# Performance work log

Hardware: AMD Instinct MI355X
Metric: run time of the kernel (lower is better)

Reference implementation:

```python
import jax, jax.numpy as jnp
import numpy as np

B, S, D, E, K = 4, 4096, 2048, 64, 2


def setup_inputs() -> dict:
    key = jax.random.key(0)
    k1, k2, k3 = jax.random.split(key, 3)
    x = jax.random.normal(k1, (B, S, D), dtype=jnp.float32)
    W = jax.random.normal(k2, (D, E), dtype=jnp.float32) / np.sqrt(D)
    b = jnp.zeros((E,), dtype=jnp.float32)
    noise = jax.random.normal(k3, (B, S, E), dtype=jnp.float32)
    return {"x": x, "W": W, "b": b, "noise": noise}


def reference(x, W, b, noise):
    # logits = Linear(x); noisy gating adds N(0,1)/10 noise
    logits = jnp.einsum('bsd,de->bse', x, W) + b  # [B,S,E]
    logits = logits + noise * 0.1
    scores = jax.nn.softmax(logits, axis=-1)      # [B,S,E]
    topk_scores, topk_indices = jax.lax.top_k(scores, K)  # [B,S,K]
    return topk_scores, topk_indices, scores
```

## Files before the change

### kernel.cpp

```cpp
#include <hip/hip_runtime.h>
#include <math.h>

#define BS_TOT 16384
#define DDIM   2048
#define NEXP   64
#define TOPK   2

#define NW   16
#define RPB  64
#define DS   (DDIM / NW)

__global__ __launch_bounds__(1024, 2)
void router_kernel(const float* __restrict__ x, const float* __restrict__ W,
                   const float* __restrict__ bias, const float* __restrict__ noise,
                   float* __restrict__ out)
{
    __shared__ float lacc[RPB][NEXP + 1];

    const int tid  = threadIdx.x;
    const int lane = tid & 63;
    const int wv   = __builtin_amdgcn_readfirstlane(tid >> 6);
    const int row0 = blockIdx.x * RPB;
    const int row  = row0 + lane;

    for (int i = tid; i < RPB * (NEXP + 1); i += 1024) ((float*)lacc)[i] = 0.0f;
    __syncthreads();

    float acc[NEXP];
#pragma unroll
    for (int e = 0; e < NEXP; ++e) acc[e] = 0.0f;

    const int d0 = wv * DS;
    const float* xp = x + (size_t)row * DDIM + d0;
    const float* Wp = W + (size_t)d0 * NEXP;

#pragma unroll 1
    for (int dd = 0; dd < DS; dd += 4) {
        const float4 xv = *(const float4*)(xp + dd);
        const float* wr = Wp + (size_t)dd * NEXP;
#pragma unroll
        for (int e = 0; e < NEXP; ++e) acc[e] = fmaf(xv.x, wr[e],            acc[e]);
#pragma unroll
        for (int e = 0; e < NEXP; ++e) acc[e] = fmaf(xv.y, wr[NEXP + e],     acc[e]);
#pragma unroll
        for (int e = 0; e < NEXP; ++e) acc[e] = fmaf(xv.z, wr[2 * NEXP + e], acc[e]);
#pragma unroll
        for (int e = 0; e < NEXP; ++e) acc[e] = fmaf(xv.w, wr[3 * NEXP + e], acc[e]);
    }

#pragma unroll
    for (int e = 0; e < NEXP; ++e) atomicAdd(&lacc[lane][e], acc[e]);
    __syncthreads();

    const float blane = bias[lane];
    float* const scores_out = out + 2 * BS_TOT * TOPK;
    float* const iout       = out + BS_TOT * TOPK;

#pragma unroll
    for (int j = 0; j < RPB / NW; ++j) {
        const int rl  = wv * (RPB / NW) + j;
        const int r2  = row0 + rl;
        const float v = lacc[rl][lane] + blane + 0.1f * noise[(size_t)r2 * NEXP + lane];

        float m = v;
#pragma unroll
        for (int off = 1; off < 64; off <<= 1) m = fmaxf(m, __shfl_xor(m, off));
        const float p = __expf(v - m);
        float s = p;
#pragma unroll
        for (int off = 1; off < 64; off <<= 1) s += __shfl_xor(s, off);
        const float sc = p * (1.0f / s);

        scores_out[(size_t)r2 * NEXP + lane] = sc;

        float a1 = v, a2 = -INFINITY;
        int   i1 = lane, i2 = 0x7fffffff;
#pragma unroll
        for (int off = 1; off < 64; off <<= 1) {
            const float o1 = __shfl_xor(a1, off), o2 = __shfl_xor(a2, off);
            const int  oi1 = __shfl_xor(i1, off), oi2 = __shfl_xor(i2, off);
            if (o1 > a1 || (o1 == a1 && oi1 < i1)) {
                if (a1 > o2 || (a1 == o2 && i1 < oi2)) { a2 = a1; i2 = i1; }
                else                                   { a2 = o2; i2 = oi2; }
                a1 = o1; i1 = oi1;
            } else {
                if (o1 > a2 || (o1 == a2 && oi1 < i2)) { a2 = o1; i2 = oi1; }
            }
        }
        const float s1 = __shfl(sc, i1);
        const float s2 = __shfl(sc, i2);
        if (lane == 0) {
            out[(size_t)r2 * TOPK + 0]  = s1;
            out[(size_t)r2 * TOPK + 1]  = s2;
            iout[(size_t)r2 * TOPK + 0] = (float)i1;
            iout[(size_t)r2 * TOPK + 1] = (float)i2;
        }
    }
}

extern "C" void kernel_launch(void* const* d_in, const int* in_sizes, int n_in,
                              void* d_out, int out_size, void* d_ws, size_t ws_size,
                              hipStream_t stream)
{
    const float* x     = (const float*)d_in[0];
    const float* W     = (const float*)d_in[1];
    const float* bias  = (const float*)d_in[2];
    const float* noise = (const float*)d_in[3];
    float* out = (float*)d_out;
    (void)in_sizes; (void)n_in; (void)out_size; (void)d_ws; (void)ws_size;

    hipLaunchKernelGGL(router_kernel, dim3(BS_TOT / RPB), dim3(1024), 0, stream,
                       x, W, bias, noise, out);
}
```

Before: 325.9 us.

## Stage x and W tiles in per-wave LDS and compute 8x8 register outer products

Replaces the per-lane row-times-W scalar loop, where every lane streams all 64 W columns through scalar or broadcast loads, with a per-wave LDS staging scheme. Each wave stages an 8-wide k-slice of x (transposed) and of W into shared memory and computes an 8x8 rows-by-experts outer-product tile per lane. Global loads for the next tile are prefetched into registers. The goal is more FMAs per load and less register pressure than the 64-accumulator layout. In exchange the kernel drops the 2-blocks-per-CU launch bound, adds LDS traffic, and has no barrier between LDS writes and reads within a wave, so it relies on wave-synchronous execution.

```diff
diff --git a/kernel.cpp b/kernel.cpp
--- a/kernel.cpp
+++ b/kernel.cpp
@@ -6,50 +6,90 @@
 #define NEXP   64
 #define TOPK   2
 
-#define NW   16
-#define RPB  64
-#define DS   (DDIM / NW)
+#define NW     16
+#define RPB    64
+#define DSLICE (DDIM / NW)
+#define TK     8
+#define NTILE  (DSLICE / TK)
 
-__global__ __launch_bounds__(1024, 2)
+__global__ __launch_bounds__(1024)
 void router_kernel(const float* __restrict__ x, const float* __restrict__ W,
                    const float* __restrict__ bias, const float* __restrict__ noise,
                    float* __restrict__ out)
 {
-    __shared__ float lacc[RPB][NEXP + 1];
+    __shared__ float smem[NW][2][TK][NEXP];
+    float (*lacc)[NEXP + 1] = (float (*)[NEXP + 1])smem;
 
     const int tid  = threadIdx.x;
     const int lane = tid & 63;
     const int wv   = __builtin_amdgcn_readfirstlane(tid >> 6);
     const int row0 = blockIdx.x * RPB;
-    const int row  = row0 + lane;
+    const int rg   = lane >> 3;
+    const int er   = lane & 7;
 
+    float acc[8][8];
+#pragma unroll
+    for (int i = 0; i < 8; ++i)
+#pragma unroll
+        for (int j = 0; j < 8; ++j) acc[i][j] = 0.0f;
+
+    const int dw0 = wv * DSLICE;
+    const float* xg = x + (size_t)(row0 + lane) * DDIM + dw0;
+    const int    wk = lane >> 3;
+    const int    we = (lane & 7) * 8;
+    const float* wg = W + (size_t)(dw0 + wk) * NEXP + we;
+
+    float4 gx0 = *(const float4*)(xg);
+    float4 gx1 = *(const float4*)(xg + 4);
+    float4 gw0 = *(const float4*)(wg);
+    float4 gw1 = *(const float4*)(wg + 4);
+
+#pragma unroll 1
+    for (int t = 0; t < NTILE; ++t) {
+        smem[wv][0][0][lane] = gx0.x;
+        smem[wv][0][1][lane] = gx0.y;
+        smem[wv][0][2][lane] = gx0.z;
+        smem[wv][0][3][lane] = gx0.w;
+        smem[wv][0][4][lane] = gx1.x;
+        smem[wv][0][5][lane] = gx1.y;
+        smem[wv][0][6][lane] = gx1.z;
+        smem[wv][0][7][lane] = gx1.w;
+        *(float4*)&smem[wv][1][wk][we]     = gw0;
+        *(float4*)&smem[wv][1][wk][we + 4] = gw1;
+
+        if (t + 1 < NTILE) {
+            const float* xn = xg + (t + 1) * TK;
+            gx0 = *(const float4*)(xn);
+            gx1 = *(const float4*)(xn + 4);
+            const float* wn = wg + (size_t)(t + 1) * TK * NEXP;
+            gw0 = *(const float4*)(wn);
+            gw1 = *(const float4*)(wn + 4);
+        }
+
+#pragma unroll 1
+        for (int k = 0; k < TK; ++k) {
+            const float4 a0 = *(const float4*)&smem[wv][0][k][rg * 8];
+            const float4 a1 = *(const float4*)&smem[wv][0][k][rg * 8 + 4];
+            const float4 b0 = *(const float4*)&smem[wv][1][k][er * 8];
+            const float4 b1 = *(const float4*)&smem[wv][1][k][er * 8 + 4];
+            const float av[8] = {a0.x, a0.y, a0.z, a0.w, a1.x, a1.y, a1.z, a1.w};
+            const float bv[8] = {b0.x, b0.y, b0.z, b0.w, b1.x, b1.y, b1.z, b1.w};
+#pragma unroll
+            for (int i = 0; i < 8; ++i)
+#pragma unroll
+                for (int j = 0; j < 8; ++j)
+                    acc[i][j] = fmaf(av[i], bv[j], acc[i][j]);
+        }
+    }
+
+    __syncthreads();
     for (int i = tid; i < RPB * (NEXP + 1); i += 1024) ((float*)lacc)[i] = 0.0f;
     __syncthreads();
-
-    float acc[NEXP];
 #pragma unroll
-    for (int e = 0; e < NEXP; ++e) acc[e] = 0.0f;
-
-    const int d0 = wv * DS;
-    const float* xp = x + (size_t)row * DDIM + d0;
-    const float* Wp = W + (size_t)d0 * NEXP;
-
-#pragma unroll 1
-    for (int dd = 0; dd < DS; dd += 4) {
-        const float4 xv = *(const float4*)(xp + dd);
-        const float* wr = Wp + (size_t)dd * NEXP;
+    for (int i = 0; i < 8; ++i)
 #pragma unroll
-        for (int e = 0; e < NEXP; ++e) acc[e] = fmaf(xv.x, wr[e],            acc[e]);
-#pragma unroll
-        for (int e = 0; e < NEXP; ++e) acc[e] = fmaf(xv.y, wr[NEXP + e],     acc[e]);
-#pragma unroll
-        for (int e = 0; e < NEXP; ++e) acc[e] = fmaf(xv.z, wr[2 * NEXP + e], acc[e]);
-#pragma unroll
-        for (int e = 0; e < NEXP; ++e) acc[e] = fmaf(xv.w, wr[3 * NEXP + e], acc[e]);
-    }
-
-#pragma unroll
-    for (int e = 0; e < NEXP; ++e) atomicAdd(&lacc[lane][e], acc[e]);
+        for (int j = 0; j < 8; ++j)
+            atomicAdd(&lacc[rg * 8 + i][er * 8 + j], acc[i][j]);
     __syncthreads();
 
     const float blane = bias[lane];
```

Measured after the change: 312.1 us. -4.3%, faster.
